# Performance work log

Hardware: AMD Instinct MI355X
Metric: run time of the kernel (lower is better)

Reference implementation:

```python
import jax, jax.numpy as jnp
import numpy as np

S, A = 8, 2
SA = S + A
N = 256


def setup_inputs() -> dict:
    key = jax.random.key(0)
    ks = jax.random.split(key, 8)
    mean_full = jax.random.normal(ks[0], (SA,), dtype=jnp.float32)
    C = jax.random.normal(ks[1], (SA, SA), dtype=jnp.float32)
    cov_full = (C @ C.T) / SA + 0.1 * jnp.eye(SA, dtype=jnp.float32)  # PSD input covariance
    dynamics_inputs = jax.random.normal(ks[2], (N, SA), dtype=jnp.float32)
    dynamics_outputs = jax.random.normal(ks[3], (N, S), dtype=jnp.float32)
    eq_coeff = 0.5 + 0.5 * jax.random.uniform(ks[4], (S,), dtype=jnp.float32)
    eq_scales = 0.5 + 0.5 * jax.random.uniform(ks[5], (S, SA), dtype=jnp.float32)
    eq_noise_coeff = 1e-2 + 1e-2 * jax.random.uniform(ks[6], (S,), dtype=jnp.float32)
    return {
        'mean_full': mean_full,
        'cov_full': cov_full,
        'dynamics_inputs': dynamics_inputs,
        'dynamics_outputs': dynamics_outputs,
        'eq_coeff': eq_coeff,
        'eq_scales': eq_scales,
        'eq_noise_coeff': eq_noise_coeff,
    }


def _eq_kernel_log(x, x_, eq_coeff, eq_scales):
    # x: [n, d], x_: [m, d] -> [S, n, m] log kernel
    diffs = x[:, None, :] - x_[None, :, :]
    quads = jnp.einsum('nmd,nmd,gd->gnm', diffs, diffs, 1.0 / eq_scales)
    return jnp.log(eq_coeff)[:, None, None] - 0.5 * quads


def reference(mean_full, cov_full, dynamics_inputs, dynamics_outputs,
              eq_coeff, eq_scales, eq_noise_coeff):
    s_dim = eq_coeff.shape[0]
    sa = mean_full.shape[0]
    n = dynamics_inputs.shape[0]
    dtype = mean_full.dtype
    mean_full = mean_full.reshape(1, sa)
    cov_full = cov_full.reshape(sa, sa)
    inv_scales = 1.0 / eq_scales  # [S, SA]
    eye_sa = jnp.eye(sa, dtype=dtype)

    # data covariance K + noise: [S, N, N]
    log_K = _eq_kernel_log(dynamics_inputs, dynamics_inputs, eq_coeff, eq_scales)
    data_cov = jnp.exp(log_K) + eq_noise_coeff[:, None, None] * eye_sa[None, :n, :n] if n == sa else jnp.exp(log_K) + eq_noise_coeff[:, None, None] * jnp.eye(n, dtype=dtype)[None]
    # beta: [S, N]
    beta = jnp.linalg.solve(data_cov, dynamics_outputs.T[:, :, None])[:, :, 0]

    # mean determinant coefficient: det(cov_full diag(1/scales_g) + I)^(-1/2)
    M = cov_full[None, :, :] * inv_scales[:, None, :] + eye_sa[None]  # [S, SA, SA]
    mean_det_coeff = eq_coeff * jnp.linalg.det(M) ** (-0.5)  # [S]

    cov_full_plus_scales = cov_full[None] + jax.vmap(jnp.diag)(eq_scales)  # [S, SA, SA]
    nu = dynamics_inputs - mean_full  # [N, SA]
    sol = jnp.linalg.solve(cov_full_plus_scales,
                           jnp.broadcast_to(nu.T[None], (s_dim, sa, n)))  # [S, SA, N]
    mean_quad = jnp.einsum('id,gdi->gi', nu, sol)
    mean_exp_quad = mean_det_coeff[:, None] * jnp.exp(-0.5 * mean_quad)  # [S, N]
    mean = jnp.einsum('gi,gi->g', beta, mean_exp_quad)  # [S]

    # R_ab = cov_full (inv_a + inv_b) + I: [S, S, SA, SA]
    cross = inv_scales[:, None, :] + inv_scales[None, :, :]  # [S, S, SA]
    R = cov_full[None, None, :, :] * cross[:, :, None, :] + eye_sa[None, None]
    _, log_R_det = jnp.linalg.slogdet(R)
    log_R_det_inv_sqrt = -0.5 * log_R_det  # [S, S]

    log_k_data_mu = _eq_kernel_log(mean_full, dynamics_inputs, eq_coeff, eq_scales)  # [S, 1, N]
    log_k_ab = log_k_data_mu[None, :, :, :] + log_k_data_mu[:, :, :, None]  # [S, S, N, N]

    eq_scale_times_nu = nu[None, :, :] * inv_scales[:, None, :]  # [S, N, SA]
    z = (eq_scale_times_nu[:, None, :, None, :] +
         eq_scale_times_nu[None, :, None, :, :])  # [S, S, N, N, SA]
    # R^{-1} cov_full, then quadratic form z^T (R^{-1} cov_full) z
    R_inv = jnp.linalg.inv(R)  # [S, S, SA, SA]
    M_ab = jnp.einsum('abij,jk->abik', R_inv, cov_full)  # [S, S, SA, SA]
    cov_quad = 0.5 * jnp.einsum('abnmi,abij,abnmj->abnm', z, M_ab, z)

    log_Q = log_k_ab + cov_quad + log_R_det_inv_sqrt[:, :, None, None]
    Q = jnp.exp(log_Q)  # [S, S, N, N]

    Q_diag = Q[jnp.arange(s_dim), jnp.arange(s_dim)]  # [S, N, N]
    expected_var = eq_coeff - jnp.trace(jnp.linalg.solve(data_cov, Q_diag),
                                        axis1=-2, axis2=-1)  # [S]

    cov = jnp.einsum('ai,bj,abij->ab', beta, beta, Q)
    cov = cov - mean[:, None] * mean[None, :]
    cov = cov + jnp.diag(expected_var)

    # input-output cross covariance
    A_inv_mean = jnp.linalg.solve(cov_full_plus_scales,
                                  jnp.broadcast_to(mean_full.T[None], (s_dim, sa, 1)))  # [S, SA, 1]
    A_inv_dyn = jnp.linalg.solve(cov_full_plus_scales,
                                 jnp.broadcast_to(dynamics_inputs.T[None], (s_dim, sa, n)))  # [S, SA, N]
    cross_cov_mu = eq_scales[:, :, None] * A_inv_mean + jnp.einsum('ij,gjk->gik', cov_full, A_inv_dyn)
    cross_cov = jnp.einsum('gk,gdk,gk->dg', mean_exp_quad, cross_cov_mu, beta)  # [SA, S]
    cross_cov_s = cross_cov[:s_dim, :] - mean_full[:, :s_dim].T * mean[None, :]

    mean = mean + mean_full[0, :s_dim]
    cov = cov + cov_full[:s_dim, :s_dim]
    cov = cov + cross_cov_s + cross_cov_s.T
    return mean, cov
```

## Files before the change

kernel.cpp:

```cpp
#include <hip/hip_runtime.h>
#include <math.h>

#define S_DIM 8
#define SA_DIM 10
#define NN 256

constexpr size_t OFF_K     = 0;
constexpr size_t OFF_LINV  = OFF_K    + 8ull*NN*NN;
constexpr size_t OFF_KINV  = OFF_LINV + 8ull*NN*NN;
constexpr size_t OFF_RD    = OFF_KINV + 8ull*NN*NN;
constexpr size_t OFF_U     = OFF_RD   + 8*NN;
constexpr size_t OFF_LK    = OFF_U    + 8*NN*SA_DIM;
constexpr size_t OFF_M     = OFF_LK   + 8*NN;
constexpr size_t OFF_C     = OFF_M    + 64*100;
constexpr size_t OFF_AINV  = OFF_C    + 64;
constexpr size_t OFF_AIM   = OFF_AINV + 800;
constexpr size_t OFF_MDC   = OFF_AIM  + 80;
constexpr size_t OFF_BETA  = OFF_MDC  + 8;
constexpr size_t OFF_MEAN  = OFF_BETA + 8*NN;
constexpr size_t OFF_CROSS = OFF_MEAN + 8;
constexpr size_t OFF_COVP  = OFF_CROSS+ 80;
constexpr size_t OFF_TRP   = OFF_COVP + 512;

__device__ void gj_invert10(float A[SA_DIM][SA_DIM], float B[SA_DIM][SA_DIM], float* logdet) {
#pragma unroll
  for (int i = 0; i < SA_DIM; i++)
#pragma unroll
    for (int j = 0; j < SA_DIM; j++) B[i][j] = (i == j) ? 1.f : 0.f;
  float ld = 0.f;
#pragma unroll
  for (int k = 0; k < SA_DIM; k++) {
    float pv = A[k][k];
    ld += logf(pv);
    float ip = 1.f / pv;
#pragma unroll
    for (int j = 0; j < SA_DIM; j++) { A[k][j] *= ip; B[k][j] *= ip; }
#pragma unroll
    for (int r = 0; r < SA_DIM; r++) {
      if (r == k) continue;
      float f = A[r][k];
#pragma unroll
      for (int j = 0; j < SA_DIM; j++) { A[r][j] -= f * A[k][j]; B[r][j] -= f * B[k][j]; }
    }
  }
  *logdet = ld;
}

__global__ __launch_bounds__(256) void k_front(const float* __restrict__ x,
                                               const float* __restrict__ mf,
                                               const float* __restrict__ cov,
                                               const float* __restrict__ eqc,
                                               const float* __restrict__ scales,
                                               const float* __restrict__ noise,
                                               float* __restrict__ Kw,
                                               float* __restrict__ u,
                                               float* __restrict__ lkw,
                                               float* __restrict__ Mw, float* __restrict__ cvec,
                                               float* __restrict__ Ainvw, float* __restrict__ aimw,
                                               float* __restrict__ mdcw) {
  int blk = blockIdx.x;
  if (blk < 2048) {
    int g = blk >> 8;
    int n = blk & 255;
    int m = threadIdx.x;
    __shared__ float xs[NN * SA_DIM];
    __shared__ float isc[SA_DIM];
    for (int i = threadIdx.x; i < NN * SA_DIM; i += 256) xs[i] = x[i];
    if (threadIdx.x < SA_DIM) isc[threadIdx.x] = 1.0f / scales[g * SA_DIM + threadIdx.x];
    __syncthreads();
    float quad = 0.f;
#pragma unroll
    for (int d = 0; d < SA_DIM; d++) {
      float df = xs[n * SA_DIM + d] - xs[m * SA_DIM + d];
      quad += df * df * isc[d];
    }
    float v = eqc[g] * __expf(-0.5f * quad);
    if (m == n) v += noise[g];
    Kw[(size_t)g * NN * NN + (size_t)n * NN + m] = v;
  } else if (blk < 2056) {
    int g = blk - 2048;
    int n = threadIdx.x;
    float quad = 0.f;
#pragma unroll
    for (int d = 0; d < SA_DIM; d++) {
      float isc = 1.0f / scales[g * SA_DIM + d];
      float nu = x[n * SA_DIM + d] - mf[d];
      u[((size_t)g * NN + n) * SA_DIM + d] = nu * isc;
      quad += nu * nu * isc;
    }
    lkw[g * NN + n] = logf(eqc[g]) - 0.5f * quad;
  } else {
    int p = threadIdx.x;
    if (p >= 64) return;
    int a = p >> 3, b = p & 7;
    float A[SA_DIM][SA_DIM], B[SA_DIM][SA_DIM];
    for (int i = 0; i < SA_DIM; i++)
      for (int j = 0; j < SA_DIM; j++)
        A[i][j] = cov[i * SA_DIM + j] * (1.f / scales[a * SA_DIM + j] + 1.f / scales[b * SA_DIM + j]) +
                  ((i == j) ? 1.f : 0.f);
    float ld;
    gj_invert10(A, B, &ld);
    cvec[p] = -0.5f * ld;
    for (int i = 0; i < SA_DIM; i++)
      for (int j = 0; j < SA_DIM; j++) {
        float v = 0.f;
        for (int k = 0; k < SA_DIM; k++) v += B[i][k] * cov[k * SA_DIM + j];
        Mw[p * 100 + i * SA_DIM + j] = v;
      }
    if (b == 0) {
      int g = a;
      for (int i = 0; i < SA_DIM; i++)
        for (int j = 0; j < SA_DIM; j++)
          A[i][j] = cov[i * SA_DIM + j] + ((i == j) ? scales[g * SA_DIM + j] : 0.f);
      float ld2;
      gj_invert10(A, B, &ld2);
      for (int i = 0; i < SA_DIM; i++)
        for (int j = 0; j < SA_DIM; j++) Ainvw[g * 100 + i * SA_DIM + j] = B[i][j];
      for (int i = 0; i < SA_DIM; i++) {
        float v = 0.f;
        for (int j = 0; j < SA_DIM; j++) v += B[i][j] * mf[j];
        aimw[g * SA_DIM + i] = v;
      }
      for (int i = 0; i < SA_DIM; i++)
        for (int j = 0; j < SA_DIM; j++)
          A[i][j] = cov[i * SA_DIM + j] * (1.f / scales[g * SA_DIM + j]) + ((i == j) ? 1.f : 0.f);
      float ld3;
      gj_invert10(A, B, &ld3);
      mdcw[g] = eqc[g] * __expf(-0.5f * ld3);
    }
  }
}

__device__ __forceinline__ void tile_idx(int tau, int ntile, int nt4, int c0,
                                         int& ib, int& jb, int& iq, int& jq) {
  int rt = ntile - 1 - tau;
  int q = (int)((sqrtf((float)(8 * rt + 1)) - 1.0f) * 0.5f);
  while ((q + 1) * (q + 2) / 2 <= rt) q++;
  while (q * (q + 1) / 2 > rt) q--;
  jq = nt4 - 1 - q;
  int rem = rt - q * (q + 1) / 2;
  iq = nt4 - 1 - rem;
  jb = c0 + 16 + 4 * jq;
  ib = c0 + 16 + 4 * iq;
}

__device__ __forceinline__ void chol_factor_panel(float* __restrict__ Ag,
                                                  float* __restrict__ rdg,
                                                  int c0, int nb, int t, int lane,
                                                  bool fromGlobal,
                                                  const float (*SRC)[248],
                                                  float (*Pdst)[248]) {
  int rr = lane & 15;
  float a[16];
  float myrs = 0.f;
  if (fromGlobal) {
#pragma unroll
    for (int j = 0; j < 16; j++)
      a[j] = (j <= rr) ? Ag[(size_t)(c0 + j) * NN + (c0 + rr)]
                       : Ag[(size_t)(c0 + rr) * NN + (c0 + j)];
  } else {
#pragma unroll
    for (int j = 0; j < 16; j++)
      a[j] = (j <= rr) ? SRC[j][rr] : SRC[rr][j];
  }
#pragma unroll
  for (int k = 0; k < 16; k++) {
    float d = __shfl(a[k], k);
    float rs_ = rsqrtf(d);
    if (rr == k) myrs = rs_;
    float m = a[k] * rs_;
#pragma unroll
    for (int j = 0; j < 16; j++) {
      if (j > k) {
        float Lkj = __shfl(a[j], k) * rs_;
        a[j] = fmaf(-m, Lkj, a[j]);
      }
    }
    a[k] = m;
  }
  if (t < 16) {
    rdg[c0 + rr] = myrs;
#pragma unroll
    for (int j = 0; j < 16; j++)
      if (j <= rr) Ag[(size_t)(c0 + j) * NN + (c0 + rr)] = a[j];
  }
  if (t < nb) {
    int i = c0 + 16 + t;
    float xs[16];
#pragma unroll
    for (int c = 0; c < 16; c++) {
      float x = fromGlobal ? Ag[(size_t)(c0 + c) * NN + i] : SRC[c][16 + t];
#pragma unroll
      for (int cp = 0; cp < 16; cp++) {
        if (cp < c) {
          float Lccp = __shfl(a[cp], c);
          x = fmaf(-Lccp, xs[cp], x);
        }
      }
      xs[c] = x * __shfl(myrs, c);
    }
#pragma unroll
    for (int c = 0; c < 16; c++) {
      Ag[(size_t)(c0 + c) * NN + i] = xs[c];
      Pdst[c][t] = xs[c];
    }
  }
}

__global__ __launch_bounds__(1024, 4) void k_chol11(float* __restrict__ Aw,
                                                    float* __restrict__ rd) {
  int g = blockIdx.x;
  float* Ag = Aw + (size_t)g * NN * NN;
  float* rdg = rd + g * NN;
  int t = threadIdx.x;
  int lane = t & 63;
  int w = t >> 6;
  __shared__ __align__(16) float P[2][16][248];
  __shared__ __align__(16) float NP[16][248];

  if (w < 4)
    chol_factor_panel(Ag, rdg, 0, 240, t, lane, true, nullptr, P[0]);
  __syncthreads();

  for (int p = 0; p < 15; p++) {
    int c0 = 16 * p;
    int nb = NN - c0 - 16;
    int nt4 = nb >> 2;
    const float (*Pc)[248] = P[p & 1];
    int ncrit = 4 * nt4 - 6;
    if (t < ncrit) {
      int jq, iq;
      if (t < nt4) { jq = 0; iq = t; }
      else if (t < 2 * nt4 - 1) { jq = 1; iq = t - nt4 + 1; }
      else if (t < 3 * nt4 - 3) { jq = 2; iq = t - (2 * nt4 - 1) + 2; }
      else { jq = 3; iq = t - (3 * nt4 - 3) + 3; }
      int jb = c0 + 16 + 4 * jq, ib = c0 + 16 + 4 * iq;
      float4 cv0 = *(const float4*)(Ag + (size_t)(jb + 0) * NN + ib);
      float4 cv1 = *(const float4*)(Ag + (size_t)(jb + 1) * NN + ib);
      float4 cv2 = *(const float4*)(Ag + (size_t)(jb + 2) * NN + ib);
      float4 cv3 = *(const float4*)(Ag + (size_t)(jb + 3) * NN + ib);
      float4 a0 = make_float4(0.f, 0.f, 0.f, 0.f), a1 = a0, a2 = a0, a3 = a0;
#pragma unroll
      for (int k = 0; k < 16; k++) {
        float4 pi = *(const float4*)(&Pc[k][4 * iq]);
        float4 pj = *(const float4*)(&Pc[k][4 * jq]);
        a0.x = fmaf(pj.x, pi.x, a0.x); a0.y = fmaf(pj.x, pi.y, a0.y);
        a0.z = fmaf(pj.x, pi.z, a0.z); a0.w = fmaf(pj.x, pi.w, a0.w);
        a1.x = fmaf(pj.y, pi.x, a1.x); a1.y = fmaf(pj.y, pi.y, a1.y);
        a1.z = fmaf(pj.y, pi.z, a1.z); a1.w = fmaf(pj.y, pi.w, a1.w);
        a2.x = fmaf(pj.z, pi.x, a2.x); a2.y = fmaf(pj.z, pi.y, a2.y);
        a2.z = fmaf(pj.z, pi.z, a2.z); a2.w = fmaf(pj.z, pi.w, a2.w);
        a3.x = fmaf(pj.w, pi.x, a3.x); a3.y = fmaf(pj.w, pi.y, a3.y);
        a3.z = fmaf(pj.w, pi.z, a3.z); a3.w = fmaf(pj.w, pi.w, a3.w);
      }
      cv0.x -= a0.x; cv0.y -= a0.y; cv0.z -= a0.z; cv0.w -= a0.w;
      cv1.x -= a1.x; cv1.y -= a1.y; cv1.z -= a1.z; cv1.w -= a1.w;
      cv2.x -= a2.x; cv2.y -= a2.y; cv2.z -= a2.z; cv2.w -= a2.w;
      cv3.x -= a3.x; cv3.y -= a3.y; cv3.z -= a3.z; cv3.w -= a3.w;
      *(float4*)(&NP[4 * jq + 0][4 * iq]) = cv0;
      *(float4*)(&NP[4 * jq + 1][4 * iq]) = cv1;
      *(float4*)(&NP[4 * jq + 2][4 * iq]) = cv2;
      *(float4*)(&NP[4 * jq + 3][4 * iq]) = cv3;
    }
    __syncthreads();
    if (w < 4) {
      chol_factor_panel(Ag, rdg, c0 + 16, nb - 16, t, lane, false, NP, P[(p + 1) & 1]);
    } else {
      int nt4b = nt4 - 4;
      int ntileB = nt4b * (nt4b + 1) / 2;
      int tau = t - 256;
      if (tau < ntileB) {
        int ib, jb, iq, jq;
        tile_idx(tau, ntileB, nt4b, c0 + 16, ib, jb, iq, jq);
        float4 cv0 = *(const float4*)(Ag + (size_t)(jb + 0) * NN + ib);
        float4 cv1 = *(const float4*)(Ag + (size_t)(jb + 1) * NN + ib);
        float4 cv2 = *(const float4*)(Ag + (size_t)(jb + 2) * NN + ib);
        float4 cv3 = *(const float4*)(Ag + (size_t)(jb + 3) * NN + ib);
        while (true) {
          int tau2 = tau + 768;
          bool h2 = tau2 < ntileB;
          int ib2 = 0, jb2 = 0, iq2 = 0, jq2 = 0;
          float4 n0, n1, n2, n3;
          if (h2) {
            tile_idx(tau2, ntileB, nt4b, c0 + 16, ib2, jb2, iq2, jq2);
            n0 = *(const float4*)(Ag + (size_t)(jb2 + 0) * NN + ib2);
            n1 = *(const float4*)(Ag + (size_t)(jb2 + 1) * NN + ib2);
            n2 = *(const float4*)(Ag + (size_t)(jb2 + 2) * NN + ib2);
            n3 = *(const float4*)(Ag + (size_t)(jb2 + 3) * NN + ib2);
          }
          float4 a0 = make_float4(0.f, 0.f, 0.f, 0.f), a1 = a0, a2 = a0, a3 = a0;
#pragma unroll
          for (int k = 0; k < 16; k++) {
            float4 pi = *(const float4*)(&Pc[k][16 + 4 * iq]);
            float4 pj = *(const float4*)(&Pc[k][16 + 4 * jq]);
            a0.x = fmaf(pj.x, pi.x, a0.x); a0.y = fmaf(pj.x, pi.y, a0.y);
            a0.z = fmaf(pj.x, pi.z, a0.z); a0.w = fmaf(pj.x, pi.w, a0.w);
            a1.x = fmaf(pj.y, pi.x, a1.x); a1.y = fmaf(pj.y, pi.y, a1.y);
            a1.z = fmaf(pj.y, pi.z, a1.z); a1.w = fmaf(pj.y, pi.w, a1.w);
            a2.x = fmaf(pj.z, pi.x, a2.x); a2.y = fmaf(pj.z, pi.y, a2.y);
            a2.z = fmaf(pj.z, pi.z, a2.z); a2.w = fmaf(pj.z, pi.w, a2.w);
            a3.x = fmaf(pj.w, pi.x, a3.x); a3.y = fmaf(pj.w, pi.y, a3.y);
            a3.z = fmaf(pj.w, pi.z, a3.z); a3.w = fmaf(pj.w, pi.w, a3.w);
          }
          cv0.x -= a0.x; cv0.y -= a0.y; cv0.z -= a0.z; cv0.w -= a0.w;
          cv1.x -= a1.x; cv1.y -= a1.y; cv1.z -= a1.z; cv1.w -= a1.w;
          cv2.x -= a2.x; cv2.y -= a2.y; cv2.z -= a2.z; cv2.w -= a2.w;
          cv3.x -= a3.x; cv3.y -= a3.y; cv3.z -= a3.z; cv3.w -= a3.w;
          *(float4*)(Ag + (size_t)(jb + 0) * NN + ib) = cv0;
          *(float4*)(Ag + (size_t)(jb + 1) * NN + ib) = cv1;
          *(float4*)(Ag + (size_t)(jb + 2) * NN + ib) = cv2;
          *(float4*)(Ag + (size_t)(jb + 3) * NN + ib) = cv3;
          if (!h2) break;
          tau = tau2; ib = ib2; jb = jb2; iq = iq2; jq = jq2;
          cv0 = n0; cv1 = n1; cv2 = n2; cv3 = n3;
        }
      }
    }
    __syncthreads();
  }
}

__global__ __launch_bounds__(256) void k_linv2(const float* __restrict__ LT,
                                               const float* __restrict__ rd,
                                               float* __restrict__ Linv) {
  int g = blockIdx.x >> 2;
  int q = blockIdx.x & 3;
  int w = threadIdx.x >> 6;
  int lane = threadIdx.x & 63;
  int j = 4 * q + w;
  const float* Ag = LT + (size_t)g * NN * NN;
  const float* rdg = rd + g * NN;
  float* Og = Linv + (size_t)g * NN * NN;
  __shared__ __align__(16) float Xl[4][16][16][16];
  __shared__ __align__(16) float Dv[16][16][16];
  int r = lane & 15, cq = lane >> 4;

  for (int s = 0; s < 4; s++) {
    int i = w + 4 * s;
    for (int e = lane; e < 256; e += 64) {
      int k = e >> 4, rr = e & 15;
      Xl[w][s][k][rr] = Ag[(size_t)(16 * i + k) * NN + 16 * i + rr];
    }
    asm volatile("s_waitcnt lgkmcnt(0)" ::: "memory");
    __builtin_amdgcn_sched_barrier(0);
    int c = lane & 15;
    float xv[16];
#pragma unroll
    for (int rr = 0; rr < 16; rr++) {
      float tmp = (rr == c) ? 1.f : 0.f;
#pragma unroll
      for (int m = 0; m < 16; m++) {
        if (m < rr) tmp = fmaf(-Xl[w][s][m][rr], xv[m], tmp);
      }
      xv[rr] = tmp * rdg[16 * i + rr];
    }
    if (lane < 16) {
#pragma unroll
      for (int rr = 0; rr < 16; rr++) Dv[i][rr][lane] = xv[rr];
    }
  }
  __syncthreads();

  {
    float4 dj = *(const float4*)&Dv[j][r][4 * cq];
    *(float4*)&Xl[w][j][r][4 * cq] = dj;
    *(float4*)(Og + (size_t)(16 * j + r) * NN + 16 * j + 4 * cq) = dj;
    float4 z = make_float4(0.f, 0.f, 0.f, 0.f);
    for (int i2 = 0; i2 < j; i2++)
      *(float4*)(Og + (size_t)(16 * i2 + r) * NN + 16 * j + 4 * cq) = z;
  }
  asm volatile("s_waitcnt lgkmcnt(0)" ::: "memory");
  __builtin_amdgcn_sched_barrier(0);

  for (int i = j + 1; i < 16; i++) {
    float4 acc = make_float4(0.f, 0.f, 0.f, 0.f);
    for (int k = j; k < i; k++) {
      const float* Lbase = Ag + (size_t)(16 * k) * NN + 16 * i + r;
      const float* Xk = &Xl[w][k][0][4 * cq];
#pragma unroll
      for (int m = 0; m < 16; m++) {
        float lv = Lbase[(size_t)m * NN];
        float4 xvv = *(const float4*)(Xk + 16 * m);
        acc.x = fmaf(lv, xvv.x, acc.x);
        acc.y = fmaf(lv, xvv.y, acc.y);
        acc.z = fmaf(lv, xvv.z, acc.z);
        acc.w = fmaf(lv, xvv.w, acc.w);
      }
    }
    float4 o = make_float4(0.f, 0.f, 0.f, 0.f);
#pragma unroll
    for (int m = 0; m < 16; m++) {
      float d = Dv[i][r][m];
      float sx = __shfl(acc.x, m + 16 * cq);
      float sy = __shfl(acc.y, m + 16 * cq);
      float sz = __shfl(acc.z, m + 16 * cq);
      float sw = __shfl(acc.w, m + 16 * cq);
      o.x = fmaf(-d, sx, o.x);
      o.y = fmaf(-d, sy, o.y);
      o.z = fmaf(-d, sz, o.z);
      o.w = fmaf(-d, sw, o.w);
    }
    *(float4*)&Xl[w][i][r][4 * cq] = o;
    *(float4*)(Og + (size_t)(16 * i + r) * NN + 16 * j + 4 * cq) = o;
    asm volatile("s_waitcnt lgkmcnt(0)" ::: "memory");
    __builtin_amdgcn_sched_barrier(0);
  }
}

__global__ __launch_bounds__(256) void k_syrk(const float* __restrict__ Linv,
                                              float* __restrict__ Kinv) {
  int g = blockIdx.x >> 4;
  int tile = blockIdx.x & 15;
  int i0 = (tile >> 2) * 64, j0 = (tile & 3) * 64;
  const float* A = Linv + (size_t)g * NN * NN;
  float* O = Kinv + (size_t)g * NN * NN;
  __shared__ float sa[32][64], sb[32][64];
  int tx = threadIdx.x & 15, ty = threadIdx.x >> 4;
  float acc[4][4] = {{0.f}};
  for (int k0 = 0; k0 < NN; k0 += 32) {
    for (int e = threadIdx.x; e < 2048; e += 256) {
      int kk = e >> 6, cc = e & 63;
      sa[kk][cc] = A[(size_t)(k0 + kk) * NN + i0 + cc];
      sb[kk][cc] = A[(size_t)(k0 + kk) * NN + j0 + cc];
    }
    __syncthreads();
#pragma unroll 8
    for (int kk = 0; kk < 32; kk++) {
      float av[4], bv[4];
#pragma unroll
      for (int q = 0; q < 4; q++) { av[q] = sa[kk][ty * 4 + q]; bv[q] = sb[kk][tx * 4 + q]; }
#pragma unroll
      for (int q = 0; q < 4; q++)
#pragma unroll
        for (int r = 0; r < 4; r++) acc[q][r] += av[q] * bv[r];
    }
    __syncthreads();
  }
#pragma unroll
  for (int q = 0; q < 4; q++)
#pragma unroll
    for (int r = 0; r < 4; r++)
      O[(size_t)(i0 + ty * 4 + q) * NN + j0 + tx * 4 + r] = acc[q][r];
}

__global__ __launch_bounds__(256) void k_beta(const float* __restrict__ Kinv,
                                              const float* __restrict__ y,
                                              float* __restrict__ betaw) {
  int g = blockIdx.x, n = threadIdx.x;
  __shared__ __align__(16) float ys[NN];
  ys[n] = y[n * S_DIM + g];
  __syncthreads();
  const float4* Kg = (const float4*)(Kinv + (size_t)g * NN * NN + (size_t)n * NN);
  float acc = 0.f;
  for (int m4 = 0; m4 < 64; m4++) {
    float4 kv = Kg[m4];
    float4 yv = ((const float4*)ys)[m4];
    acc += kv.x * yv.x + kv.y * yv.y + kv.z * yv.z + kv.w * yv.w;
  }
  betaw[g * NN + n] = acc;
}

__global__ __launch_bounds__(256) void k_back(const float* __restrict__ u,
                                              const float* __restrict__ lkw,
                                              const float* __restrict__ Mw,
                                              const float* __restrict__ cvec,
                                              const float* __restrict__ Kinv,
                                              const float* __restrict__ betaw,
                                              const float* __restrict__ x,
                                              const float* __restrict__ mf,
                                              const float* __restrict__ cov,
                                              const float* __restrict__ scales,
                                              const float* __restrict__ Ainvw,
                                              const float* __restrict__ aimw,
                                              const float* __restrict__ mdcw,
                                              float* __restrict__ covp, float* __restrict__ trp,
                                              float* __restrict__ meanw, float* __restrict__ crossw) {
  int blk = blockIdx.x;
  int t = threadIdx.x;
  if (blk < 512) {
    int p = blk >> 3;
    int eighth = blk & 7;
    int a = p >> 3, b = p & 7;
    __shared__ __align__(16) float ub[NN * 12];
    __shared__ float Ms[100];
    __shared__ float sbv[NN];
    __shared__ float eb[NN];
    __shared__ float red[256];
    {
      const float* ur = u + (size_t)b * NN * SA_DIM + (size_t)t * SA_DIM;
      float* ud = &ub[t * 12];
#pragma unroll
      for (int d = 0; d < SA_DIM; d++) ud[d] = ur[d];
    }
    if (t < 100) Ms[t] = Mw[p * 100 + t];
    eb[t] = betaw[b * NN + t];
    __syncthreads();
    {
      const float* um = &ub[t * 12];
      float qd = 0.f;
#pragma unroll
      for (int d = 0; d < SA_DIM; d++) {
        float v = 0.f;
#pragma unroll
        for (int e = 0; e < SA_DIM; e++) v += Ms[d * SA_DIM + e] * um[e];
        qd += v * um[d];
      }
      sbv[t] = lkw[b * NN + t] + 0.5f * qd;
    }
    __syncthreads();
    int n = eighth * 32 + (t >> 3);
    int c = t & 7;
    float ua[SA_DIM];
#pragma unroll
    for (int d = 0; d < SA_DIM; d++) ua[d] = u[((size_t)a * NN + n) * SA_DIM + d];
    float va[SA_DIM];
#pragma unroll
    for (int d = 0; d < SA_DIM; d++) {
      float v = 0.f;
#pragma unroll
      for (int e = 0; e < SA_DIM; e++) v += Ms[d * SA_DIM + e] * ua[e];
      va[d] = v;
    }
    float qa = 0.f;
#pragma unroll
    for (int d = 0; d < SA_DIM; d++) qa += va[d] * ua[d];
    float pa = lkw[a * NN + n] + 0.5f * qa + cvec[p];
    float wa = betaw[a * NN + n];
    const float* Krow = Kinv + (size_t)a * NN * NN + (size_t)n * NN;
    float covacc = 0.f, tracc = 0.f;
    bool dg = (a == b);
    for (int ii = 0; ii < 32; ii++) {
      int mm = c + 8 * ii;
      const float* ur = &ub[mm * 12];
      float4 f0 = *(const float4*)ur;
      float4 f1 = *(const float4*)(ur + 4);
      float4 f2 = *(const float4*)(ur + 8);
      float s = pa + sbv[mm];
      s += va[0] * f0.x + va[1] * f0.y + va[2] * f0.z + va[3] * f0.w;
      s += va[4] * f1.x + va[5] * f1.y + va[6] * f1.z + va[7] * f1.w;
      s += va[8] * f2.x + va[9] * f2.y;
      float e = __expf(s);
      covacc += eb[mm] * e;
      if (dg) tracc += Krow[mm] * e;
    }
    covacc *= wa;
    red[t] = covacc;
    __syncthreads();
    for (int st = 128; st > 0; st >>= 1) {
      if (t < st) red[t] += red[t + st];
      __syncthreads();
    }
    if (t == 0) covp[blk] = red[0];
    if (dg) {
      red[t] = tracc;
      __syncthreads();
      for (int st = 128; st > 0; st >>= 1) {
        if (t < st) red[t] += red[t + st];
        __syncthreads();
      }
      if (t == 0) trp[a * 8 + eighth] = red[0];
    }
  } else {
    int g = blk - 512;
    int i = t;
    __shared__ float Ai[100], cv[100], aims[SA_DIM], sc[SA_DIM], mfs[SA_DIM];
    __shared__ float red[256];
    if (i < 100) { Ai[i] = Ainvw[g * 100 + i]; cv[i] = cov[i]; }
    if (i < SA_DIM) { aims[i] = aimw[g * SA_DIM + i]; sc[i] = scales[g * SA_DIM + i]; mfs[i] = mf[i]; }
    __syncthreads();
    float bg = betaw[g * NN + i];
    float xi[SA_DIM], nu[SA_DIM];
#pragma unroll
    for (int d = 0; d < SA_DIM; d++) { xi[d] = x[i * SA_DIM + d]; nu[d] = xi[d] - mfs[d]; }
    float sv[SA_DIM], ad[SA_DIM];
#pragma unroll
    for (int d = 0; d < SA_DIM; d++) {
      float s1 = 0.f, s2 = 0.f;
#pragma unroll
      for (int e = 0; e < SA_DIM; e++) { s1 += Ai[d * SA_DIM + e] * nu[e]; s2 += Ai[d * SA_DIM + e] * xi[e]; }
      sv[d] = s1;
      ad[d] = s2;
    }
    float mq = 0.f;
#pragma unroll
    for (int d = 0; d < SA_DIM; d++) mq += nu[d] * sv[d];
    float mexp = mdcw[g] * __expf(-0.5f * mq);
    float cm = bg * mexp;
    float contrib[SA_DIM];
#pragma unroll
    for (int d = 0; d < SA_DIM; d++) {
      float ccm = sc[d] * aims[d];
#pragma unroll
      for (int jj = 0; jj < SA_DIM; jj++) ccm += cv[d * SA_DIM + jj] * ad[jj];
      contrib[d] = mexp * ccm * bg;
    }
    red[i] = cm;
    __syncthreads();
    for (int st = 128; st > 0; st >>= 1) {
      if (i < st) red[i] += red[i + st];
      __syncthreads();
    }
    if (i == 0) meanw[g] = red[0];
    for (int d = 0; d < SA_DIM; d++) {
      __syncthreads();
      red[i] = contrib[d];
      __syncthreads();
      for (int st = 128; st > 0; st >>= 1) {
        if (i < st) red[i] += red[i + st];
        __syncthreads();
      }
      if (i == 0) crossw[d * S_DIM + g] = red[0];
    }
  }
}

__global__ __launch_bounds__(64) void k_final(const float* __restrict__ covp,
                                              const float* __restrict__ trp,
                                              const float* __restrict__ meanw,
                                              const float* __restrict__ crossw,
                                              const float* __restrict__ cov,
                                              const float* __restrict__ eqc,
                                              const float* __restrict__ mf,
                                              float* __restrict__ out) {
  int p = threadIdx.x;
  if (p >= 64) return;
  int a = p >> 3, b = p & 7;
  float covq = 0.f;
#pragma unroll
  for (int e = 0; e < 8; e++) covq += covp[p * 8 + e];
  float ma = meanw[a], mb = meanw[b];
  float val = covq - ma * mb + cov[a * SA_DIM + b];
  if (a == b) {
    float tr = 0.f;
#pragma unroll
    for (int e = 0; e < 8; e++) tr += trp[a * 8 + e];
    val += eqc[a] - tr;
  }
  val += (crossw[a * S_DIM + b] - mf[a] * mb) + (crossw[b * S_DIM + a] - mf[b] * ma);
  out[S_DIM + p] = val;
  if (p < S_DIM) out[p] = meanw[p] + mf[p];
}

extern "C" void kernel_launch(void* const* d_in, const int* in_sizes, int n_in,
                              void* d_out, int out_size, void* d_ws, size_t ws_size,
                              hipStream_t stream) {
  const float* mf     = (const float*)d_in[0];
  const float* cov    = (const float*)d_in[1];
  const float* x      = (const float*)d_in[2];
  const float* y      = (const float*)d_in[3];
  const float* eqc    = (const float*)d_in[4];
  const float* scales = (const float*)d_in[5];
  const float* noise  = (const float*)d_in[6];
  float* ws = (float*)d_ws;

  float* Kw    = ws + OFF_K;
  float* Linv  = ws + OFF_LINV;
  float* Kinv  = ws + OFF_KINV;
  float* rd    = ws + OFF_RD;
  float* u     = ws + OFF_U;
  float* lkw   = ws + OFF_LK;
  float* Mw    = ws + OFF_M;
  float* cvec  = ws + OFF_C;
  float* Ainvw = ws + OFF_AINV;
  float* aimw  = ws + OFF_AIM;
  float* mdcw  = ws + OFF_MDC;
  float* betaw = ws + OFF_BETA;
  float* meanw = ws + OFF_MEAN;
  float* crossw= ws + OFF_CROSS;
  float* covp  = ws + OFF_COVP;
  float* trp   = ws + OFF_TRP;

  k_front<<<2057, 256, 0, stream>>>(x, mf, cov, eqc, scales, noise, Kw, u, lkw, Mw, cvec,
                                    Ainvw, aimw, mdcw);
  k_chol11<<<8, 1024, 0, stream>>>(Kw, rd);
  k_linv2<<<32, 256, 0, stream>>>(Kw, rd, Linv);
  k_syrk<<<128, 256, 0, stream>>>(Linv, Kinv);
  k_beta<<<8, 256, 0, stream>>>(Kinv, y, betaw);
  k_back<<<520, 256, 0, stream>>>(u, lkw, Mw, cvec, Kinv, betaw, x, mf, cov, scales,
                                  Ainvw, aimw, mdcw, covp, trp, meanw, crossw);
  k_final<<<1, 64, 0, stream>>>(covp, trp, meanw, crossw, cov, eqc, mf, (float*)d_out);
}
```

Measured before the change: 271.0 us.

## Exploit symmetry in SYRK and move Cholesky panel writeback to all threads

```diff
diff --git a/kernel.cpp b/kernel.cpp
--- a/kernel.cpp
+++ b/kernel.cpp
@@ -186,10 +186,11 @@
   }
   if (t < nb) {
     int i = c0 + 16 + t;
+    (void)i;
     float xs[16];
 #pragma unroll
     for (int c = 0; c < 16; c++) {
-      float x = fromGlobal ? Ag[(size_t)(c0 + c) * NN + i] : SRC[c][16 + t];
+      float x = fromGlobal ? Ag[(size_t)(c0 + c) * NN + (c0 + 16 + t)] : SRC[c][16 + t];
 #pragma unroll
       for (int cp = 0; cp < 16; cp++) {
         if (cp < c) {
@@ -200,14 +201,12 @@
       xs[c] = x * __shfl(myrs, c);
     }
 #pragma unroll
-    for (int c = 0; c < 16; c++) {
-      Ag[(size_t)(c0 + c) * NN + i] = xs[c];
+    for (int c = 0; c < 16; c++)
       Pdst[c][t] = xs[c];
-    }
-  }
-}
-
-__global__ __launch_bounds__(1024, 4) void k_chol11(float* __restrict__ Aw,
+  }
+}
+
+__global__ __launch_bounds__(1024, 4) void k_chol13(float* __restrict__ Aw,
                                                     float* __restrict__ rd) {
   int g = blockIdx.x;
   float* Ag = Aw + (size_t)g * NN * NN;
@@ -261,6 +260,15 @@
       *(float4*)(&NP[4 * jq + 1][4 * iq]) = cv1;
       *(float4*)(&NP[4 * jq + 2][4 * iq]) = cv2;
       *(float4*)(&NP[4 * jq + 3][4 * iq]) = cv3;
+    }
+    {
+      int nb4 = nb >> 2;
+      int tot = 16 * nb4;
+      for (int e = t; e < tot; e += 1024) {
+        int c = e / nb4, s4 = e - c * nb4;
+        float4 v = *(const float4*)(&Pc[c][4 * s4]);
+        *(float4*)(Ag + (size_t)(c0 + c) * NN + c0 + 16 + 4 * s4) = v;
+      }
     }
     __syncthreads();
     if (w < 4) {
@@ -407,32 +415,40 @@
   }
 }
 
-__global__ __launch_bounds__(256) void k_syrk(const float* __restrict__ Linv,
-                                              float* __restrict__ Kinv) {
-  int g = blockIdx.x >> 4;
-  int tile = blockIdx.x & 15;
-  int i0 = (tile >> 2) * 64, j0 = (tile & 3) * 64;
+__global__ __launch_bounds__(256) void k_syrk2(const float* __restrict__ Linv,
+                                               float* __restrict__ Kinv) {
+  int g = blockIdx.x / 10;
+  int tile = blockIdx.x - g * 10;
+  int ti = 0, rem = tile;
+  while (rem >= 4 - ti) { rem -= 4 - ti; ti++; }
+  int tj = ti + rem;
+  int i0 = ti * 64, j0 = tj * 64;
   const float* A = Linv + (size_t)g * NN * NN;
   float* O = Kinv + (size_t)g * NN * NN;
-  __shared__ float sa[32][64], sb[32][64];
+  __shared__ __align__(16) float smem[4096];
+  float* sa = smem;
+  float* sb = smem + 2048;
   int tx = threadIdx.x & 15, ty = threadIdx.x >> 4;
   float acc[4][4] = {{0.f}};
   for (int k0 = 0; k0 < NN; k0 += 32) {
     for (int e = threadIdx.x; e < 2048; e += 256) {
       int kk = e >> 6, cc = e & 63;
-      sa[kk][cc] = A[(size_t)(k0 + kk) * NN + i0 + cc];
-      sb[kk][cc] = A[(size_t)(k0 + kk) * NN + j0 + cc];
+      sa[kk * 64 + cc] = A[(size_t)(k0 + kk) * NN + i0 + cc];
+      sb[kk * 64 + cc] = A[(size_t)(k0 + kk) * NN + j0 + cc];
     }
     __syncthreads();
 #pragma unroll 8
     for (int kk = 0; kk < 32; kk++) {
-      float av[4], bv[4];
-#pragma unroll
-      for (int q = 0; q < 4; q++) { av[q] = sa[kk][ty * 4 + q]; bv[q] = sb[kk][tx * 4 + q]; }
-#pragma unroll
-      for (int q = 0; q < 4; q++)
-#pragma unroll
-        for (int r = 0; r < 4; r++) acc[q][r] += av[q] * bv[r];
+      float4 av = *(const float4*)(&sa[kk * 64 + ty * 4]);
+      float4 bv = *(const float4*)(&sb[kk * 64 + tx * 4]);
+      acc[0][0] = fmaf(av.x, bv.x, acc[0][0]); acc[0][1] = fmaf(av.x, bv.y, acc[0][1]);
+      acc[0][2] = fmaf(av.x, bv.z, acc[0][2]); acc[0][3] = fmaf(av.x, bv.w, acc[0][3]);
+      acc[1][0] = fmaf(av.y, bv.x, acc[1][0]); acc[1][1] = fmaf(av.y, bv.y, acc[1][1]);
+      acc[1][2] = fmaf(av.y, bv.z, acc[1][2]); acc[1][3] = fmaf(av.y, bv.w, acc[1][3]);
+      acc[2][0] = fmaf(av.z, bv.x, acc[2][0]); acc[2][1] = fmaf(av.z, bv.y, acc[2][1]);
+      acc[2][2] = fmaf(av.z, bv.z, acc[2][2]); acc[2][3] = fmaf(av.z, bv.w, acc[2][3]);
+      acc[3][0] = fmaf(av.w, bv.x, acc[3][0]); acc[3][1] = fmaf(av.w, bv.y, acc[3][1]);
+      acc[3][2] = fmaf(av.w, bv.z, acc[3][2]); acc[3][3] = fmaf(av.w, bv.w, acc[3][3]);
     }
     __syncthreads();
   }
@@ -441,6 +457,21 @@
 #pragma unroll
     for (int r = 0; r < 4; r++)
       O[(size_t)(i0 + ty * 4 + q) * NN + j0 + tx * 4 + r] = acc[q][r];
+  if (ti != tj) {
+    __syncthreads();
+#pragma unroll
+    for (int q = 0; q < 4; q++)
+#pragma unroll
+      for (int r = 0; r < 4; r++)
+        smem[(ty * 4 + q) * 64 + tx * 4 + r] = acc[q][r];
+    __syncthreads();
+    for (int e = threadIdx.x; e < 1024; e += 256) {
+      int rr = e >> 4, c4 = (e & 15) * 4;
+      float4 v = make_float4(smem[(c4 + 0) * 64 + rr], smem[(c4 + 1) * 64 + rr],
+                             smem[(c4 + 2) * 64 + rr], smem[(c4 + 3) * 64 + rr]);
+      *(float4*)(O + (size_t)(j0 + rr) * NN + i0 + c4) = v;
+    }
+  }
 }
 
 __global__ __launch_bounds__(256) void k_beta(const float* __restrict__ Kinv,
@@ -672,9 +703,9 @@
 
   k_front<<<2057, 256, 0, stream>>>(x, mf, cov, eqc, scales, noise, Kw, u, lkw, Mw, cvec,
                                     Ainvw, aimw, mdcw);
-  k_chol11<<<8, 1024, 0, stream>>>(Kw, rd);
+  k_chol13<<<8, 1024, 0, stream>>>(Kw, rd);
   k_linv2<<<32, 256, 0, stream>>>(Kw, rd, Linv);
-  k_syrk<<<128, 256, 0, stream>>>(Linv, Kinv);
+  k_syrk2<<<80, 256, 0, stream>>>(Linv, Kinv);
   k_beta<<<8, 256, 0, stream>>>(Kinv, y, betaw);
   k_back<<<520, 256, 0, stream>>>(u, lkw, Mw, cvec, Kinv, betaw, x, mf, cov, scales,
                                   Ainvw, aimw, mdcw, covp, trp, meanw, crossw);
```

New measurement: 275.9 us. About the same (+1.8%).
